# Optimization experiments

Hardware: AMD Instinct MI355X
Metric: run time of the kernel (lower is better)

Reference implementation:

```python
import jax, jax.numpy as jnp
import numpy as np

EPS = 1e-5
D_MODEL = 1024
NUM_HEADS = 16
D_HEAD = D_MODEL // NUM_HEADS


def _exp_map(v, c):
    # (1/sqrt(c)) * tanh(sqrt(c)*||v||) * v/||v||
    sqrt_c = jnp.sqrt(c)
    n = jnp.maximum(jnp.linalg.norm(v, axis=-1, keepdims=True), EPS)
    return jnp.tanh(sqrt_c * n) / (sqrt_c * n) * v


def _log_map(y, c):
    sqrt_c = jnp.sqrt(c)
    n = jnp.maximum(jnp.linalg.norm(y, axis=-1, keepdims=True), EPS)
    n_cl = jnp.minimum(n, 1.0 / sqrt_c - EPS)
    return jnp.arctanh(sqrt_c * n_cl) / (sqrt_c * n) * y


def _poincare_distance(x, y, c):
    # x, y: (B, H, N, d). Returns (B, H, N, N).
    xns = jnp.sum(x * x, axis=-1, keepdims=True)          # (B,H,N,1)
    yns = jnp.sum(y * y, axis=-1, keepdims=True)          # (B,H,N,1)
    dot = jnp.einsum('bhnd,bhmd->bhnm', x, y)             # (B,H,N,N)
    yns_t = jnp.swapaxes(yns, -1, -2)                     # (B,H,1,N)
    diff_sq = xns - 2.0 * dot + yns_t
    denom = (1.0 - c * xns) * (1.0 - c * yns_t)
    arg = 1.0 + 2.0 * c * diff_sq / jnp.maximum(denom, EPS)
    return jnp.arccosh(jnp.maximum(arg, 1.0 + EPS)) / jnp.sqrt(c)


def setup_inputs() -> dict:
    key = jax.random.key(0)
    ks = jax.random.split(key, 6)
    B, N = 1, 2048
    x = jax.random.normal(ks[0], (B, N, D_MODEL), dtype=jnp.float32)
    s = 0.02
    W_q = jax.random.normal(ks[1], (D_MODEL, D_MODEL), dtype=jnp.float32) * s
    W_k = jax.random.normal(ks[2], (D_MODEL, D_MODEL), dtype=jnp.float32) * s
    W_v = jax.random.normal(ks[3], (D_MODEL, D_MODEL), dtype=jnp.float32) * s
    W_o = jax.random.normal(ks[4], (D_MODEL, D_MODEL), dtype=jnp.float32) * s
    mask = jnp.tril(jnp.ones((N, N), dtype=bool))[None, None]  # (1,1,N,N) causal
    return {
        'x': x, 'W_q': W_q, 'W_k': W_k, 'W_v': W_v, 'W_o': W_o,
        'log_c': jnp.float32(0.0), 'beta': jnp.float32(0.0),
        'attention_bias': jnp.float32(0.0), 'mask': mask,
    }


def reference(x, W_q, W_k, W_v, W_o, log_c, beta, attention_bias, mask):
    B, N, _ = x.shape
    c = jax.nn.softplus(log_c)
    # nn.Linear(bias=False): y = x @ W.T
    q_t = (x @ W_q.T).reshape(B, N, NUM_HEADS, D_HEAD).transpose(0, 2, 1, 3)
    k_t = (x @ W_k.T).reshape(B, N, NUM_HEADS, D_HEAD).transpose(0, 2, 1, 3)
    v_t = (x @ W_v.T).reshape(B, N, NUM_HEADS, D_HEAD).transpose(0, 2, 1, 3)
    # map q, k onto the Poincare ball
    q = _exp_map(q_t, c)
    k = _exp_map(k_t, c)
    dist = _poincare_distance(q, k, c)                    # (B,H,N,N)
    beta_pos = jax.nn.softplus(beta)
    scores = -beta_pos * dist - attention_bias
    neg_big = -jnp.finfo(jnp.float32).max
    scores = jnp.where(mask, scores, neg_big)
    weights = jax.nn.softmax(scores, axis=-1)
    out_tangent = jnp.einsum('bhnm,bhmd->bhnd', weights, v_t)
    out_hyper = _exp_map(out_tangent, c)
    out_tangent_heads = _log_map(out_hyper, c)
    concat = out_tangent_heads.transpose(0, 2, 1, 3).reshape(B, N, D_MODEL)
    return concat @ W_o.T
```

## Files before the change

### kernel.cpp

```cpp
#include <hip/hip_runtime.h>
#include <stdint.h>

#define EPSF 1e-5f

typedef float f32x4 __attribute__((ext_vector_type(4)));
typedef short bf16x8 __attribute__((ext_vector_type(8)));

__device__ __forceinline__ float softplus_f(float x) {
    return x > 20.f ? x : log1pf(expf(x));
}

__device__ __forceinline__ unsigned short f2bf(float f) {
    union { float f; unsigned int u; } v; v.f = f;
    unsigned int r = v.u + 0x7FFFu + ((v.u >> 16) & 1u);
    return (unsigned short)(r >> 16);
}
__device__ __forceinline__ float bf2f(unsigned short u) {
    union { unsigned int i; float f; } v; v.i = ((unsigned int)u) << 16;
    return v.f;
}
__device__ __forceinline__ int cvt_pk_bf16(float a, float b) {
    int d;
    asm("v_cvt_pk_bf16_f32 %0, %1, %2" : "=v"(d) : "v"(a), "v"(b));
    return d;
}
__device__ __forceinline__ int bperm(int byte_addr, int v) {
    return __builtin_amdgcn_ds_bpermute(byte_addr, v);
}
__device__ __forceinline__ float bpermf(int byte_addr, float v) {
    return __int_as_float(__builtin_amdgcn_ds_bpermute(byte_addr, __float_as_int(v)));
}
__device__ __forceinline__ float rcp_f(float x)  { float d; asm("v_rcp_f32 %0, %1"  : "=v"(d) : "v"(x)); return d; }
__device__ __forceinline__ float sqrt_f(float x) { float d; asm("v_sqrt_f32 %0, %1" : "=v"(d) : "v"(x)); return d; }
__device__ __forceinline__ float log2_f(float x) { float d; asm("v_log_f32 %0, %1"  : "=v"(d) : "v"(x)); return d; }
__device__ __forceinline__ float exp2_f(float x) { float d; asm("v_exp_f32 %0, %1"  : "=v"(d) : "v"(x)); return d; }

__global__ __launch_bounds__(256) void k_f2b_all(const float* __restrict__ x,
                                                 const float* __restrict__ W0, const float* __restrict__ W1,
                                                 const float* __restrict__ W2, const float* __restrict__ W3,
                                                 unsigned short* __restrict__ xb,
                                                 unsigned short* __restrict__ o0, unsigned short* __restrict__ o1,
                                                 unsigned short* __restrict__ o2, unsigned short* __restrict__ o3) {
    const int NX4 = 524288;
    const int NW4 = 262144;
    int i = blockIdx.x * 256 + threadIdx.x;
    int stride = gridDim.x * 256;
    for (; i < NX4 + 4 * NW4; i += stride) {
        const float4* src;
        ushort4* dst;
        if (i < NX4) {
            src = (const float4*)x + i;
            dst = (ushort4*)xb + i;
        } else {
            int j = i - NX4;
            int sel = j >> 18, off = j & (NW4 - 1);
            const float* s = sel == 0 ? W0 : sel == 1 ? W1 : sel == 2 ? W2 : W3;
            unsigned short* d = sel == 0 ? o0 : sel == 1 ? o1 : sel == 2 ? o2 : o3;
            src = (const float4*)s + off;
            dst = (ushort4*)d + off;
        }
        float4 v = *src;
        ushort4 o;
        o.x = f2bf(v.x); o.y = f2bf(v.y); o.z = f2bf(v.z); o.w = f2bf(v.w);
        *dst = o;
    }
}

#if defined(__has_builtin)
#if __has_builtin(__builtin_amdgcn_global_load_lds)
#define HAVE_GLL 1
#endif
#endif

template <int QKV>
__global__ __launch_bounds__(256) void k_gemm_gll(const unsigned short* __restrict__ A,
                                                  const unsigned short* __restrict__ B,
                                                  void* __restrict__ C0, void* __restrict__ C1,
                                                  void* __restrict__ C2,
                                                  int M, int N, int K) {
    __shared__ __align__(16) unsigned short As[128 * 32];
    __shared__ __align__(16) unsigned short Bs[64 * 32];
    const int tid  = threadIdx.x;
    const int lane = tid & 63;
    const int w    = tid >> 6;
    const int wr   = w >> 1, wc = w & 1;
    const int fr   = lane & 15;
    const int fg   = lane >> 4;
    const int nbx  = N >> 6;
    const int bx   = blockIdx.x % nbx;
    const int by   = blockIdx.x / nbx;
    const int bm0  = by * 128, bn0 = bx * 64;

    const int lrow = lane >> 2;
    const int lcol = (lane & 3) * 8;

    f32x4 acc[4][2] = {};

    for (int kk = 0; kk < K; kk += 32) {
#ifdef HAVE_GLL
        {
            const unsigned short* gp0 = &A[(size_t)(bm0 + w * 16 + lrow) * K + kk + lcol];
            __builtin_amdgcn_global_load_lds((const __attribute__((address_space(1))) void*)gp0,
                (__attribute__((address_space(3))) void*)&As[(w * 16) * 32], 16, 0, 0);
            const unsigned short* gp1 = &A[(size_t)(bm0 + 64 + w * 16 + lrow) * K + kk + lcol];
            __builtin_amdgcn_global_load_lds((const __attribute__((address_space(1))) void*)gp1,
                (__attribute__((address_space(3))) void*)&As[(64 + w * 16) * 32], 16, 0, 0);
            const unsigned short* gp2 = &B[(size_t)(bn0 + w * 16 + lrow) * K + kk + lcol];
            __builtin_amdgcn_global_load_lds((const __attribute__((address_space(1))) void*)gp2,
                (__attribute__((address_space(3))) void*)&Bs[(w * 16) * 32], 16, 0, 0);
        }
#else
        {
            uint4 a0 = *(const uint4*)&A[(size_t)(bm0 + w * 16 + lrow) * K + kk + lcol];
            uint4 a1 = *(const uint4*)&A[(size_t)(bm0 + 64 + w * 16 + lrow) * K + kk + lcol];
            uint4 b0 = *(const uint4*)&B[(size_t)(bn0 + w * 16 + lrow) * K + kk + lcol];
            *(uint4*)&As[(w * 16 + lrow) * 32 + lcol]      = a0;
            *(uint4*)&As[(64 + w * 16 + lrow) * 32 + lcol] = a1;
            *(uint4*)&Bs[(w * 16 + lrow) * 32 + lcol]      = b0;
        }
#endif
        __syncthreads();

        bf16x8 av[4], bv[2];
#pragma unroll
        for (int m = 0; m < 4; m++)
            av[m] = *(const bf16x8*)&As[(wr * 64 + m * 16 + fr) * 32 + fg * 8];
#pragma unroll
        for (int n = 0; n < 2; n++)
            bv[n] = *(const bf16x8*)&Bs[(wc * 32 + n * 16 + fr) * 32 + fg * 8];
#pragma unroll
        for (int m = 0; m < 4; m++)
#pragma unroll
            for (int n = 0; n < 2; n++)
                acc[m][n] = __builtin_amdgcn_mfma_f32_16x16x32_bf16(av[m], bv[n], acc[m][n], 0, 0, 0);
        __syncthreads();
    }

    const int crow0 = bm0 + wr * 64 + fg * 4;
    if (QKV) {
        const int sel = bn0 >> 10;
        const int lc0 = bn0 & 1023;
        unsigned short* Cp = (unsigned short*)(sel == 0 ? C0 : sel == 1 ? C1 : C2);
#pragma unroll
        for (int m = 0; m < 4; m++)
#pragma unroll
            for (int n = 0; n < 2; n++)
#pragma unroll
                for (int r = 0; r < 4; r++)
                    Cp[(size_t)(crow0 + m * 16 + r) * 1024 + lc0 + wc * 32 + n * 16 + fr] =
                        f2bf(acc[m][n][r]);
    } else {
        float* Cf = (float*)C0;
#pragma unroll
        for (int m = 0; m < 4; m++)
#pragma unroll
            for (int n = 0; n < 2; n++)
#pragma unroll
                for (int r = 0; r < 4; r++)
                    Cf[(size_t)(crow0 + m * 16 + r) * N + bn0 + wc * 32 + n * 16 + fr] =
                        acc[m][n][r];
    }
}

__global__ __launch_bounds__(256) void k_vt(const unsigned short* __restrict__ Vb,
                                            unsigned short* __restrict__ Vtg) {
    __shared__ unsigned short T[64][72];
    const int b = blockIdx.x;
    const int h = b & 15;
    const int n0 = (b >> 4) << 6;
    const int tid = threadIdx.x;
#pragma unroll
    for (int p = 0; p < 2; p++) {
        int idx = tid + p * 256;
        int r = idx >> 3, cbv = (idx & 7) * 8;
        *(uint4*)&T[r][cbv] = *(const uint4*)&Vb[(size_t)(n0 + r) * 1024 + h * 64 + cbv];
    }
    __syncthreads();
#pragma unroll
    for (int p = 0; p < 2; p++) {
        int idx = tid + p * 256;
        int d = idx >> 3, nb = (idx & 7) * 8;
        bf16x8 tv;
#pragma unroll
        for (int j = 0; j < 8; j++) tv[j] = (short)T[nb + j][d];
        *(bf16x8*)&Vtg[(size_t)(h * 64 + d) * 2048 + n0 + nb] = tv;
    }
}

__global__ __launch_bounds__(256) void k_expmap2(unsigned short* __restrict__ Qb,
                                                 unsigned short* __restrict__ Kb,
                                                 float* __restrict__ xns, float* __restrict__ xds,
                                                 float* __restrict__ yns, float* __restrict__ yds,
                                                 const float* __restrict__ pLogC) {
    float c  = softplus_f(pLogC[0]);
    float sc = sqrtf(c);
    const int bid = blockIdx.x;
    const bool isK = bid >= 8192;
    unsigned short* QK = isK ? Kb : Qb;
    float* ns = isK ? yns : xns;
    float* ds = isK ? yds : xds;
    int gid  = ((bid & 8191) * 256 + threadIdx.x) >> 6;
    int lane = threadIdx.x & 63;
    int n = gid >> 4, h = gid & 15;
    size_t idx = (size_t)n * 1024 + h * 64 + lane;
    float v  = bf2f(QK[idx]);
    float n2 = v * v;
#pragma unroll
    for (int o = 1; o < 64; o <<= 1) n2 += __shfl_xor(n2, o);
    float nn = fmaxf(sqrtf(n2), EPSF);
    float u  = sc * nn;
    float e  = __expf(-2.f * u);
    float th = (1.f - e) / (1.f + e);
    float f  = th / (sc * nn);
    QK[idx]  = f2bf(f * v);
    if (lane == 0) {
        float xn = f * f * n2;
        ns[h * 2048 + n] = xn;
        float op = 1.f + e;
        float sech2 = 4.f * e / (op * op);
        ds[h * 2048 + n] = (n2 < 1e-6f) ? (1.f - c * xn) : sech2;
    }
}

__global__ __launch_bounds__(256) void k_attn_part(const unsigned short* __restrict__ Qb,
                                                   const unsigned short* __restrict__ Kb,
                                                   const unsigned short* __restrict__ Vtg,
                                                   const float* __restrict__ xns,
                                                   const float* __restrict__ xds,
                                                   const float* __restrict__ yns,
                                                   const float* __restrict__ yds,
                                                   const float* __restrict__ pLogC,
                                                   const float* __restrict__ pBeta,
                                                   unsigned short* __restrict__ Og,
                                                   float* __restrict__ ml,
                                                   unsigned short* __restrict__ conc) {
    __shared__ __align__(16) unsigned short Ks[64][72];
    __shared__ __align__(16) unsigned short Vt[64][72];
    __shared__ __align__(16) float yl[64];
    __shared__ __align__(16) float ydl[64];

    const float c      = softplus_f(pLogC[0]);
    const float sc     = sqrtf(c);
    const float inv_sc = 1.f / sc;
    const float bpos   = softplus_f(pBeta[0]);
    const float b2     = bpos * inv_sc;
    const float twoc   = 2.f * c;
    const float m4c    = -4.f * c;

    const int b = 2303 - blockIdx.x;
    const int h = b / 144;
    const int t = b % 144;
    const int a = (t >= 4) + (t >= 12) + (t >= 24) + (t >= 40) + (t >= 60) + (t >= 84) + (t >= 112);
    const int r0_ = t - 2 * a * (a + 1);
    const int nch = a + 1;
    const int qt  = 4 * a + r0_ / nch;
    const int ci  = r0_ - (r0_ / nch) * nch;
    const int jt0 = ci * (qt + 1) / nch;
    const int jt1 = (ci + 1) * (qt + 1) / nch;
    const int q0  = qt << 6;
    const int slot = b;
    const bool full = (a == 0);

    const int tid  = threadIdx.x;
    const int lane = tid & 63;
    const int w    = tid >> 6;
    const int wq0  = w * 16;
    const int fr   = lane & 15;
    const int fg   = lane >> 4;
    const int rS   = tid >> 3;
    const int cS   = (tid & 7) * 8;

    const int qglob = q0 + wq0 + fr;
    const float xi2 = twoc * xns[h * 2048 + qglob];
    const float dxr = xds[h * 2048 + qglob];

    const unsigned short* qp = &Qb[(size_t)qglob * 1024 + h * 64 + fg * 8];
    const bf16x8 qb0 = *(const bf16x8*)qp;
    const bf16x8 qb1 = *(const bf16x8*)(qp + 32);

    float lrow = 0.f;
    f32x4 acc[4] = {};

    uint4 kr0, kr1, vr0, vr1;
    float ylr = 0.f;
#define LOAD_TILE(jtv) do { int kb = (jtv) << 6; \
    kr0 = *(const uint4*)&Kb[(size_t)(kb + rS) * 1024 + h * 64 + cS]; \
    kr1 = *(const uint4*)&Kb[(size_t)(kb + 32 + rS) * 1024 + h * 64 + cS]; \
    vr0 = *(const uint4*)&Vtg[(size_t)(h * 64 + rS) * 2048 + kb + cS]; \
    vr1 = *(const uint4*)&Vtg[(size_t)(h * 64 + 32 + rS) * 2048 + kb + cS]; \
    if (tid < 64) ylr = yns[h * 2048 + kb + tid]; \
    else if (tid < 128) ylr = yds[h * 2048 + kb + tid - 64]; \
} while (0)

#define XFORM(DOMASK) do { \
    _Pragma("unroll") for (int tn = 0; tn < 4; tn++) { \
        float4 yv  = *(const float4*)&yl[tn * 16 + fg * 4];    \
        float4 ydv = *(const float4*)&ydl[tn * 16 + fg * 4]; \
        _Pragma("unroll") for (int r = 0; r < 4; r++) { \
            float diff2 = fmaf(st[tn][r], m4c, xi2 + (&yv.x)[r]); \
            float den   = fmaxf(dxr * (&ydv.x)[r], EPSF); \
            float tt    = fmaxf(diff2 * rcp_f(den), EPSF); \
            float wv    = 1.f + tt + sqrt_f(tt * (tt + 2.f)); \
            float sv    = -b2 * log2_f(wv); \
            if (DOMASK && (k0 + tn * 16 + fg * 4 + r > qglob)) sv = -3.0e38f; \
            p[tn][r] = exp2_f(sv);            \
        } \
    } \
} while (0)

    LOAD_TILE(jt0);
    for (int jt = jt0; jt < jt1; ++jt) {
        const int k0 = jt << 6;
        __syncthreads();
        *(uint4*)&Ks[rS][cS]      = kr0;
        *(uint4*)&Ks[32 + rS][cS] = kr1;
        *(uint4*)&Vt[rS][cS]      = vr0;
        *(uint4*)&Vt[32 + rS][cS] = vr1;
        if (tid < 64)       yl[tid]       = twoc * ylr;
        else if (tid < 128) ydl[tid - 64] = ylr;
        __syncthreads();
        if (jt + 1 < jt1) LOAD_TILE(jt + 1);

        f32x4 st[4] = {};
#pragma unroll
        for (int tn = 0; tn < 4; tn++) {
            bf16x8 ka0 = *(const bf16x8*)&Ks[tn * 16 + fr][fg * 8];
            bf16x8 ka1 = *(const bf16x8*)&Ks[tn * 16 + fr][32 + fg * 8];
            st[tn] = __builtin_amdgcn_mfma_f32_16x16x32_bf16(ka0, qb0, st[tn], 0, 0, 0);
            st[tn] = __builtin_amdgcn_mfma_f32_16x16x32_bf16(ka1, qb1, st[tn], 0, 0, 0);
        }

        float p[4][4];
        if (jt == qt) XFORM(1); else XFORM(0);

        {
            float r0 = (p[0][0] + p[0][1]) + (p[0][2] + p[0][3]);
            float r1 = (p[1][0] + p[1][1]) + (p[1][2] + p[1][3]);
            float r2 = (p[2][0] + p[2][1]) + (p[2][2] + p[2][3]);
            float r3 = (p[3][0] + p[3][1]) + (p[3][2] + p[3][3]);
            lrow += (r0 + r1) + (r2 + r3);
        }

        int lo[4], hi[4];
#pragma unroll
        for (int tn = 0; tn < 4; tn++) {
            lo[tn] = cvt_pk_bf16(p[tn][0], p[tn][1]);
            hi[tn] = cvt_pk_bf16(p[tn][2], p[tn][3]);
        }
        const int adrA = (fr + ((fg & 1) << 5)) << 2;
        const int adrB = adrA + 64;
        const bool hiSel = (fg >= 2);
        union PU { int i[4]; bf16x8 v; };
        PU pu0, pu1;
#pragma unroll
        for (int kh = 0; kh < 2; kh++) {
            int l0 = bperm(adrA, lo[2 * kh]);
            int l1 = bperm(adrA, lo[2 * kh + 1]);
            int h0 = bperm(adrA, hi[2 * kh]);
            int h1 = bperm(adrA, hi[2 * kh + 1]);
            int l0b = bperm(adrB, lo[2 * kh]);
            int l1b = bperm(adrB, lo[2 * kh + 1]);
            int h0b = bperm(adrB, hi[2 * kh]);
            int h1b = bperm(adrB, hi[2 * kh + 1]);
            PU& pu = kh ? pu1 : pu0;
            pu.i[0] = hiSel ? l1 : l0;
            pu.i[1] = hiSel ? h1 : h0;
            pu.i[2] = hiSel ? l1b : l0b;
            pu.i[3] = hiSel ? h1b : h0b;
        }
        bf16x8 pa0 = pu0.v, pa1 = pu1.v;

#pragma unroll
        for (int tn = 0; tn < 4; tn++) {
            bf16x8 vb0 = *(const bf16x8*)&Vt[tn * 16 + fr][fg * 8];
            bf16x8 vb1 = *(const bf16x8*)&Vt[tn * 16 + fr][32 + fg * 8];
            acc[tn] = __builtin_amdgcn_mfma_f32_16x16x32_bf16(pa0, vb0, acc[tn], 0, 0, 0);
            acc[tn] = __builtin_amdgcn_mfma_f32_16x16x32_bf16(pa1, vb1, acc[tn], 0, 0, 0);
        }
    }
#undef LOAD_TILE
#undef XFORM

    lrow += __shfl_xor(lrow, 16);
    lrow += __shfl_xor(lrow, 32);

    if (full) {
        float lr[4];
#pragma unroll
        for (int r = 0; r < 4; r++) lr[r] = bpermf((fg * 4 + r) << 2, lrow);
#pragma unroll
        for (int r = 0; r < 4; r++) {
            float rl = 1.f / lr[r];
            float tvv[4];
            float n2 = 0.f;
#pragma unroll
            for (int tn = 0; tn < 4; tn++) { tvv[tn] = acc[tn][r] * rl; n2 += tvv[tn] * tvv[tn]; }
#pragma unroll
            for (int o = 1; o < 16; o <<= 1) n2 += __shfl_xor(n2, o);
            float nt   = fmaxf(sqrtf(n2), EPSF);
            float f1   = tanhf(sc * nt) / (sc * nt);
            float ny   = fmaxf(f1 * sqrtf(n2), EPSF);
            float ncl  = fminf(ny, inv_sc - EPSF);
            float coef = atanhf(sc * ncl) / (sc * ny);
            int row = q0 + wq0 + fg * 4 + r;
#pragma unroll
            for (int tn = 0; tn < 4; tn++)
                conc[(size_t)row * 1024 + h * 64 + tn * 16 + fr] = f2bf(coef * f1 * tvv[tn]);
        }
    } else {
        if (fg == 0)
            ml[(size_t)slot * 64 + wq0 + fr] = lrow;
#pragma unroll
        for (int r = 0; r < 4; r++) {
            int row = wq0 + fg * 4 + r;
#pragma unroll
            for (int tn = 0; tn < 4; tn++)
                Og[(size_t)slot * 4096 + row * 64 + tn * 16 + fr] = f2bf(acc[tn][r]);
        }
    }
}

__global__ __launch_bounds__(256) void k_merge(const unsigned short* __restrict__ Og,
                                               const float* __restrict__ ml,
                                               const float* __restrict__ pLogC,
                                               unsigned short* __restrict__ conc) {
    const float c      = softplus_f(pLogC[0]);
    const float sc     = sqrtf(c);
    const float inv_sc = 1.f / sc;
    int gid2 = (blockIdx.x * 256 + threadIdx.x) >> 6;
    int lane = threadIdx.x & 63;
    int h = gid2 / 1792;
    int i = 256 + (gid2 - h * 1792);
    int qt = i >> 6, row = i & 63;
    int a = qt >> 2;
    int nch = a + 1;
    int slot0 = h * 144 + 2 * a * (a + 1) + (qt & 3) * (a + 1);

    float L = 0.f, O = 0.f;
    for (int k = 0; k < nch; k++) {
        L += ml[(size_t)(slot0 + k) * 64 + row];
        O += bf2f(Og[(size_t)(slot0 + k) * 4096 + row * 64 + lane]);
    }
    float tv = O / L;
    float n2 = tv * tv;
#pragma unroll
    for (int o = 1; o < 64; o <<= 1) n2 += __shfl_xor(n2, o);
    float nt   = fmaxf(sqrtf(n2), EPSF);
    float f1   = tanhf(sc * nt) / (sc * nt);
    float ny   = fmaxf(f1 * sqrtf(n2), EPSF);
    float ncl  = fminf(ny, inv_sc - EPSF);
    float coef = atanhf(sc * ncl) / (sc * ny);
    conc[(size_t)i * 1024 + h * 64 + lane] = f2bf(coef * f1 * tv);
}

extern "C" void kernel_launch(void* const* d_in, const int* in_sizes, int n_in,
                              void* d_out, int out_size, void* d_ws, size_t ws_size,
                              hipStream_t stream) {
    const float* x     = (const float*)d_in[0];
    const float* Wq    = (const float*)d_in[1];
    const float* Wk    = (const float*)d_in[2];
    const float* Wv    = (const float*)d_in[3];
    const float* Wo    = (const float*)d_in[4];
    const float* pLogC = (const float*)d_in[5];
    const float* pBeta = (const float*)d_in[6];
    float* out = (float*)d_out;

    char* w = (char*)d_ws;
    unsigned short* Vtg   = (unsigned short*)(w);
    unsigned short* Qtb   = (unsigned short*)(w + (4u  << 20));
    unsigned short* Ktb   = (unsigned short*)(w + (8u  << 20));
    unsigned short* concb = (unsigned short*)(w + (12u << 20));
    float*          xns   = (float*)(w + (16u << 20));
    float*          yns   = (float*)(w + (16u << 20) + (1u << 17));
    float*          xds   = (float*)(w + (16u << 20) + (2u << 17));
    float*          yds   = (float*)(w + (16u << 20) + (3u << 17));
    unsigned short* wob   = (unsigned short*)(w + (16u << 20) + (1u << 19));
    unsigned short* xb    = (unsigned short*)(w + (18u << 20) + (1u << 19));
    unsigned short* wqb   = (unsigned short*)(w + (22u << 20) + (1u << 19));
    unsigned short* wkb   = (unsigned short*)(w + (24u << 20) + (1u << 19));
    unsigned short* wvb   = (unsigned short*)(w + (26u << 20) + (1u << 19));
    unsigned short* Vb    = (unsigned short*)(w + (28u << 20) + (1u << 19));
    unsigned short* Og    = (unsigned short*)(w + (18u << 20) + (1u << 19));
    float*          ml    = (float*)(w + (36u << 20) + (1u << 19));

    k_f2b_all<<<2048, 256, 0, stream>>>(x, Wq, Wk, Wv, Wo, xb, wqb, wkb, wvb, wob);

    k_gemm_gll<1><<<768, 256, 0, stream>>>(xb, wqb, Qtb, Ktb, Vb, 2048, 3072, 1024);

    k_vt<<<512, 256, 0, stream>>>(Vb, Vtg);

    k_expmap2<<<16384, 256, 0, stream>>>(Qtb, Ktb, xns, xds, yns, yds, pLogC);

    k_attn_part<<<2304, 256, 0, stream>>>(Qtb, Ktb, Vtg, xns, xds, yns, yds,
                                          pLogC, pBeta, Og, ml, concb);

    k_merge<<<7168, 256, 0, stream>>>(Og, ml, pLogC, concb);

    k_gemm_gll<0><<<256, 256, 0, stream>>>(concb, wob, out, nullptr, nullptr,
                                           2048, 1024, 1024);
}
```

Before: 146.2 us.

## Load K/V fragments directly from global in attention and shrink GEMM tiles

The attention kernel drops its LDS staging of K, V^T and the per-key norm vectors and their block-wide barriers. Each wave now reads its MFMA operand fragments straight from global memory, relying on L2/L1 caching for the reuse across the four waves. Separately, the GEMM tile is cut from 128x64 to 64x64 and the grids doubled to give more blocks per GPU. This trades barriers and LDS traffic for redundant global loads that are no longer prefetched, and the smaller GEMM tiles lower per-block operand reuse.

```diff
diff --git a/kernel.cpp b/kernel.cpp
--- a/kernel.cpp
+++ b/kernel.cpp
@@ -78,7 +78,7 @@
                                                   void* __restrict__ C0, void* __restrict__ C1,
                                                   void* __restrict__ C2,
                                                   int M, int N, int K) {
-    __shared__ __align__(16) unsigned short As[128 * 32];
+    __shared__ __align__(16) unsigned short As[64 * 32];
     __shared__ __align__(16) unsigned short Bs[64 * 32];
     const int tid  = threadIdx.x;
     const int lane = tid & 63;
@@ -89,12 +89,12 @@
     const int nbx  = N >> 6;
     const int bx   = blockIdx.x % nbx;
     const int by   = blockIdx.x / nbx;
-    const int bm0  = by * 128, bn0 = bx * 64;
+    const int bm0  = by * 64, bn0 = bx * 64;
 
     const int lrow = lane >> 2;
     const int lcol = (lane & 3) * 8;
 
-    f32x4 acc[4][2] = {};
+    f32x4 acc[2][2] = {};
 
     for (int kk = 0; kk < K; kk += 32) {
 #ifdef HAVE_GLL
@@ -102,47 +102,42 @@
             const unsigned short* gp0 = &A[(size_t)(bm0 + w * 16 + lrow) * K + kk + lcol];
             __builtin_amdgcn_global_load_lds((const __attribute__((address_space(1))) void*)gp0,
                 (__attribute__((address_space(3))) void*)&As[(w * 16) * 32], 16, 0, 0);
-            const unsigned short* gp1 = &A[(size_t)(bm0 + 64 + w * 16 + lrow) * K + kk + lcol];
+            const unsigned short* gp1 = &B[(size_t)(bn0 + w * 16 + lrow) * K + kk + lcol];
             __builtin_amdgcn_global_load_lds((const __attribute__((address_space(1))) void*)gp1,
-                (__attribute__((address_space(3))) void*)&As[(64 + w * 16) * 32], 16, 0, 0);
-            const unsigned short* gp2 = &B[(size_t)(bn0 + w * 16 + lrow) * K + kk + lcol];
-            __builtin_amdgcn_global_load_lds((const __attribute__((address_space(1))) void*)gp2,
                 (__attribute__((address_space(3))) void*)&Bs[(w * 16) * 32], 16, 0, 0);
         }
 #else
         {
             uint4 a0 = *(const uint4*)&A[(size_t)(bm0 + w * 16 + lrow) * K + kk + lcol];
-            uint4 a1 = *(const uint4*)&A[(size_t)(bm0 + 64 + w * 16 + lrow) * K + kk + lcol];
             uint4 b0 = *(const uint4*)&B[(size_t)(bn0 + w * 16 + lrow) * K + kk + lcol];
-            *(uint4*)&As[(w * 16 + lrow) * 32 + lcol]      = a0;
-            *(uint4*)&As[(64 + w * 16 + lrow) * 32 + lcol] = a1;
-            *(uint4*)&Bs[(w * 16 + lrow) * 32 + lcol]      = b0;
+            *(uint4*)&As[(w * 16 + lrow) * 32 + lcol] = a0;
+            *(uint4*)&Bs[(w * 16 + lrow) * 32 + lcol] = b0;
         }
 #endif
         __syncthreads();
 
-        bf16x8 av[4], bv[2];
-#pragma unroll
-        for (int m = 0; m < 4; m++)
-            av[m] = *(const bf16x8*)&As[(wr * 64 + m * 16 + fr) * 32 + fg * 8];
+        bf16x8 av[2], bv[2];
+#pragma unroll
+        for (int m = 0; m < 2; m++)
+            av[m] = *(const bf16x8*)&As[(wr * 32 + m * 16 + fr) * 32 + fg * 8];
 #pragma unroll
         for (int n = 0; n < 2; n++)
             bv[n] = *(const bf16x8*)&Bs[(wc * 32 + n * 16 + fr) * 32 + fg * 8];
 #pragma unroll
-        for (int m = 0; m < 4; m++)
+        for (int m = 0; m < 2; m++)
 #pragma unroll
             for (int n = 0; n < 2; n++)
                 acc[m][n] = __builtin_amdgcn_mfma_f32_16x16x32_bf16(av[m], bv[n], acc[m][n], 0, 0, 0);
         __syncthreads();
     }
 
-    const int crow0 = bm0 + wr * 64 + fg * 4;
+    const int crow0 = bm0 + wr * 32 + fg * 4;
     if (QKV) {
         const int sel = bn0 >> 10;
         const int lc0 = bn0 & 1023;
         unsigned short* Cp = (unsigned short*)(sel == 0 ? C0 : sel == 1 ? C1 : C2);
 #pragma unroll
-        for (int m = 0; m < 4; m++)
+        for (int m = 0; m < 2; m++)
 #pragma unroll
             for (int n = 0; n < 2; n++)
 #pragma unroll
@@ -152,7 +147,7 @@
     } else {
         float* Cf = (float*)C0;
 #pragma unroll
-        for (int m = 0; m < 4; m++)
+        for (int m = 0; m < 2; m++)
 #pragma unroll
             for (int n = 0; n < 2; n++)
 #pragma unroll
@@ -234,11 +229,6 @@
                                                    unsigned short* __restrict__ Og,
                                                    float* __restrict__ ml,
                                                    unsigned short* __restrict__ conc) {
-    __shared__ __align__(16) unsigned short Ks[64][72];
-    __shared__ __align__(16) unsigned short Vt[64][72];
-    __shared__ __align__(16) float yl[64];
-    __shared__ __align__(16) float ydl[64];
-
     const float c      = softplus_f(pLogC[0]);
     const float sc     = sqrtf(c);
     const float inv_sc = 1.f / sc;
@@ -267,8 +257,6 @@
     const int wq0  = w * 16;
     const int fr   = lane & 15;
     const int fg   = lane >> 4;
-    const int rS   = tid >> 3;
-    const int cS   = (tid & 7) * 8;
 
     const int qglob = q0 + wq0 + fr;
     const float xi2 = twoc * xns[h * 2048 + qglob];
@@ -278,60 +266,44 @@
     const bf16x8 qb0 = *(const bf16x8*)qp;
     const bf16x8 qb1 = *(const bf16x8*)(qp + 32);
 
+    const unsigned short* Kbase = Kb  + (size_t)fr * 1024 + h * 64 + fg * 8;
+    const unsigned short* Vbase = Vtg + (size_t)(h * 64 + fr) * 2048 + fg * 8;
+    const float* ybase  = yns + h * 2048 + fg * 4;
+    const float* ydbase = yds + h * 2048 + fg * 4;
+
     float lrow = 0.f;
     f32x4 acc[4] = {};
 
-    uint4 kr0, kr1, vr0, vr1;
-    float ylr = 0.f;
-#define LOAD_TILE(jtv) do { int kb = (jtv) << 6; \
-    kr0 = *(const uint4*)&Kb[(size_t)(kb + rS) * 1024 + h * 64 + cS]; \
-    kr1 = *(const uint4*)&Kb[(size_t)(kb + 32 + rS) * 1024 + h * 64 + cS]; \
-    vr0 = *(const uint4*)&Vtg[(size_t)(h * 64 + rS) * 2048 + kb + cS]; \
-    vr1 = *(const uint4*)&Vtg[(size_t)(h * 64 + 32 + rS) * 2048 + kb + cS]; \
-    if (tid < 64) ylr = yns[h * 2048 + kb + tid]; \
-    else if (tid < 128) ylr = yds[h * 2048 + kb + tid - 64]; \
-} while (0)
-
-#define XFORM(DOMASK) do { \
-    _Pragma("unroll") for (int tn = 0; tn < 4; tn++) { \
-        float4 yv  = *(const float4*)&yl[tn * 16 + fg * 4];    \
-        float4 ydv = *(const float4*)&ydl[tn * 16 + fg * 4]; \
-        _Pragma("unroll") for (int r = 0; r < 4; r++) { \
-            float diff2 = fmaf(st[tn][r], m4c, xi2 + (&yv.x)[r]); \
-            float den   = fmaxf(dxr * (&ydv.x)[r], EPSF); \
-            float tt    = fmaxf(diff2 * rcp_f(den), EPSF); \
-            float wv    = 1.f + tt + sqrt_f(tt * (tt + 2.f)); \
-            float sv    = -b2 * log2_f(wv); \
-            if (DOMASK && (k0 + tn * 16 + fg * 4 + r > qglob)) sv = -3.0e38f; \
-            p[tn][r] = exp2_f(sv);            \
-        } \
-    } \
-} while (0)
-
-    LOAD_TILE(jt0);
     for (int jt = jt0; jt < jt1; ++jt) {
         const int k0 = jt << 6;
-        __syncthreads();
-        *(uint4*)&Ks[rS][cS]      = kr0;
-        *(uint4*)&Ks[32 + rS][cS] = kr1;
-        *(uint4*)&Vt[rS][cS]      = vr0;
-        *(uint4*)&Vt[32 + rS][cS] = vr1;
-        if (tid < 64)       yl[tid]       = twoc * ylr;
-        else if (tid < 128) ydl[tid - 64] = ylr;
-        __syncthreads();
-        if (jt + 1 < jt1) LOAD_TILE(jt + 1);
 
         f32x4 st[4] = {};
 #pragma unroll
         for (int tn = 0; tn < 4; tn++) {
-            bf16x8 ka0 = *(const bf16x8*)&Ks[tn * 16 + fr][fg * 8];
-            bf16x8 ka1 = *(const bf16x8*)&Ks[tn * 16 + fr][32 + fg * 8];
+            const unsigned short* kr = Kbase + (size_t)(k0 + tn * 16) * 1024;
+            bf16x8 ka0 = *(const bf16x8*)kr;
+            bf16x8 ka1 = *(const bf16x8*)(kr + 32);
             st[tn] = __builtin_amdgcn_mfma_f32_16x16x32_bf16(ka0, qb0, st[tn], 0, 0, 0);
             st[tn] = __builtin_amdgcn_mfma_f32_16x16x32_bf16(ka1, qb1, st[tn], 0, 0, 0);
         }
 
         float p[4][4];
-        if (jt == qt) XFORM(1); else XFORM(0);
+        const bool diag = (jt == qt);
+#pragma unroll
+        for (int tn = 0; tn < 4; tn++) {
+            float4 ynv = *(const float4*)(ybase  + k0 + tn * 16);
+            float4 ydv = *(const float4*)(ydbase + k0 + tn * 16);
+#pragma unroll
+            for (int r = 0; r < 4; r++) {
+                float diff2 = fmaf(st[tn][r], m4c, fmaf((&ynv.x)[r], twoc, xi2));
+                float den   = fmaxf(dxr * (&ydv.x)[r], EPSF);
+                float tt    = fmaxf(diff2 * rcp_f(den), EPSF);
+                float wv    = 1.f + tt + sqrt_f(tt * (tt + 2.f));
+                float sv    = -b2 * log2_f(wv);
+                if (diag && (k0 + tn * 16 + fg * 4 + r > qglob)) sv = -3.0e38f;
+                p[tn][r] = exp2_f(sv);
+            }
+        }
 
         {
             float r0 = (p[0][0] + p[0][1]) + (p[0][2] + p[0][3]);
@@ -372,14 +344,13 @@
 
 #pragma unroll
         for (int tn = 0; tn < 4; tn++) {
-            bf16x8 vb0 = *(const bf16x8*)&Vt[tn * 16 + fr][fg * 8];
-            bf16x8 vb1 = *(const bf16x8*)&Vt[tn * 16 + fr][32 + fg * 8];
+            const unsigned short* vr = Vbase + (size_t)(tn * 16) * 2048 + k0;
+            bf16x8 vb0 = *(const bf16x8*)vr;
+            bf16x8 vb1 = *(const bf16x8*)(vr + 32);
             acc[tn] = __builtin_amdgcn_mfma_f32_16x16x32_bf16(pa0, vb0, acc[tn], 0, 0, 0);
             acc[tn] = __builtin_amdgcn_mfma_f32_16x16x32_bf16(pa1, vb1, acc[tn], 0, 0, 0);
         }
     }
-#undef LOAD_TILE
-#undef XFORM
 
     lrow += __shfl_xor(lrow, 16);
     lrow += __shfl_xor(lrow, 32);
@@ -485,7 +456,7 @@
 
     k_f2b_all<<<2048, 256, 0, stream>>>(x, Wq, Wk, Wv, Wo, xb, wqb, wkb, wvb, wob);
 
-    k_gemm_gll<1><<<768, 256, 0, stream>>>(xb, wqb, Qtb, Ktb, Vb, 2048, 3072, 1024);
+    k_gemm_gll<1><<<1536, 256, 0, stream>>>(xb, wqb, Qtb, Ktb, Vb, 2048, 3072, 1024);
 
     k_vt<<<512, 256, 0, stream>>>(Vb, Vtg);
 
@@ -496,6 +467,6 @@
 
     k_merge<<<7168, 256, 0, stream>>>(Og, ml, pLogC, concb);
 
-    k_gemm_gll<0><<<256, 256, 0, stream>>>(concb, wob, out, nullptr, nullptr,
+    k_gemm_gll<0><<<512, 256, 0, stream>>>(concb, wob, out, nullptr, nullptr,
                                            2048, 1024, 1024);
 }
```

After: 197.0 us. +34.7%, slower.
